# Kernel optimization log

Hardware: AMD Instinct MI355X
Metric: run time of the kernel (lower is better)

## Reference

```python
import jax, jax.numpy as jnp
import numpy as np

B, S, K_IN = 8, 2048, 128
D_MODEL, N_INPUT, N_PROC = 1024, 256, 1024
K_PROC = 256


def setup_inputs() -> dict:
    key = jax.random.key(0)
    k1, k2, k3, k4 = jax.random.split(key, 4)
    selected_input_acts = jax.random.normal(k1, (B, S, K_IN), dtype=jnp.float32)
    input_idx = jax.random.randint(k2, (B, K_IN), 0, N_INPUT)
    # learned params (orthogonal init in torch; random normal is fine for a numeric baseline)
    process_weights = jax.random.normal(k3, (N_PROC, N_INPUT), dtype=jnp.float32) * (2.0 / N_INPUT) ** 0.5
    process_outputs = jax.random.normal(k4, (N_PROC, D_MODEL), dtype=jnp.float32) * (2.0 / N_PROC) ** 0.5
    return {
        "selected_input_acts": selected_input_acts,
        "process_weights": process_weights,
        "process_outputs": process_outputs,
        "input_idx": input_idx,
        "k_process": K_PROC,
    }


def reference(selected_input_acts, process_weights, process_outputs, input_idx, k_process):
    # gather per-batch columns of process_weights: [B, k_input, n_process]
    sel_w = process_weights.T[input_idx]  # (N,P) indexed by (B,k) -> (B,k,P)
    # bmm + exact (erf) gelu, matching torch F.gelu default: [B, S, n_process]
    process_acts = jax.nn.gelu(
        jnp.einsum("bsk,bkp->bsp", selected_input_acts, sel_w),
        approximate=False,
    )
    # router: mean over sequence, top-k process neurons per batch
    process_scores = process_acts.mean(axis=1)  # [B, n_process]
    _, process_idx = jax.lax.top_k(process_scores, k_process)  # [B, k_process]
    # gather selected activations: [B, S, k_process]
    sel_acts = jnp.take_along_axis(process_acts, process_idx[:, None, :], axis=2)
    # gather selected output vectors: [B, k_process, d_model]
    sel_out = process_outputs[process_idx]
    # combine: [B, S, d_model]
    output = jnp.einsum("bsk,bkd->bsd", sel_acts, sel_out)
    return output
```

## Files before the change

kernel.cpp:

```cpp
#include <hip/hip_runtime.h>
#include <hip/hip_bf16.h>

#define NB    8
#define NS    2048
#define NKIN  128
#define NPROC 1024
#define NIN   256
#define NDM   1024
#define NKP   256
#define NSEG  32

typedef unsigned short u16;
typedef unsigned int   u32;
typedef __attribute__((ext_vector_type(4))) u16   u16x4;
typedef __attribute__((ext_vector_type(8))) u16   u16x8;
typedef __attribute__((ext_vector_type(4))) float f32x4;
typedef __attribute__((ext_vector_type(8))) short bf16x8;
typedef __attribute__((ext_vector_type(4))) float f32x4v;

__device__ __forceinline__ float bf2f(u16 u) {
    union { u32 i; float f; } v; v.i = ((u32)u) << 16; return v.f;
}
__device__ __forceinline__ u16 f2bf(float f) {
    u32 x = __float_as_uint(f);
    u32 r = (x + 0x7FFFu + ((x >> 16) & 1u)) >> 16;
    return (u16)r;
}
__device__ __forceinline__ float gelu_fast(float x) {
    float y  = fabsf(x) * 0.70710678118654752f;
    float t  = __builtin_amdgcn_rcpf(fmaf(0.3275911f, y, 1.0f));
    float p  = t * fmaf(t, fmaf(t, fmaf(t, fmaf(t, 1.061405429f,
               -1.453152027f), 1.421413741f), -0.284496736f), 0.254829592f);
    float e  = __expf(-y * y);
    float er = fmaf(-p, e, 1.0f);
    float s  = copysignf(er, x);
    return 0.5f * x * (1.0f + s);
}
__device__ __forceinline__ int clampi(int v, int hi) {
    return v < 0 ? 0 : (v > hi ? hi : v);
}

__global__ __launch_bounds__(256) void k0a_splitA(
        const float* __restrict__ A, u16* __restrict__ AHi,
        u16* __restrict__ ALo) {
    size_t i = ((size_t)blockIdx.x * 256 + threadIdx.x) * 8;
    if (i >= (size_t)NB * NS * NKIN) return;
    f32x4 a = *(const f32x4*)&A[i];
    f32x4 c = *(const f32x4*)&A[i + 4];
    u16x8 h, l;
    #pragma unroll
    for (int j = 0; j < 4; ++j) {
        u16 hj = f2bf(a[j]); h[j] = hj;     l[j]     = f2bf(a[j] - bf2f(hj));
        u16 hk = f2bf(c[j]); h[j + 4] = hk; l[j + 4] = f2bf(c[j] - bf2f(hk));
    }
    *(u16x8*)&AHi[i] = h;
    *(u16x8*)&ALo[i] = l;
}

__global__ __launch_bounds__(256) void k0_prep(
        const float* __restrict__ W, const int* __restrict__ idx,
        u16* __restrict__ WgHi, u16* __restrict__ WgLo) {
    const int b  = blockIdx.x;
    const int p0 = blockIdx.y * 128;
    const int tid = threadIdx.x;
    __shared__ int idxs[NKIN];
    if (tid < NKIN) idxs[tid] = clampi(idx[b * NKIN + tid], NIN - 1);
    __syncthreads();
    for (int e = tid; e < 128 * NKIN; e += 256) {
        int p = p0 + (e >> 7), k = e & 127;
        float x  = W[p * NIN + idxs[k]];
        u16 hi   = f2bf(x);
        u16 lo   = f2bf(x - bf2f(hi));
        size_t o = (size_t)(b * NPROC + p) * NKIN + k;
        WgHi[o] = hi;
        WgLo[o] = lo;
    }
}

__global__ __launch_bounds__(256) void k1_scores(
        const u16* __restrict__ AHi, const u16* __restrict__ ALo,
        const u16* __restrict__ WgHi, const u16* __restrict__ WgLo,
        float* __restrict__ scores, u16* __restrict__ acts) {
    const int lin  = blockIdx.x;
    const int b    = lin & 7;
    const int q    = lin >> 3;
    const int pblk = q & 15;
    const int sblk = q >> 4;
    const int p0 = pblk * 64, s0 = sblk * 64;
    const int tid  = threadIdx.x;
    const int lane = tid & 63;
    const int wid  = tid >> 6;
    const int wr   = wid >> 1;
    const int wc   = wid & 1;

    __shared__ u16  Ah[64 * 64], Al[64 * 64];
    __shared__ u16  Wh[64 * 64], Wl[64 * 64];
    __shared__ float red[2][64];

    f32x4v acc[2][2] = {};

    for (int kc = 0; kc < 2; ++kc) {
        __syncthreads();
        for (int e = tid; e < 512; e += 256) {
            int r = e >> 3, g = e & 7;
            size_t src = (size_t)(b * NS + s0 + r) * NKIN + kc * 64 + g * 8;
            u32 off = (u32)r * 128 + (((u32)g ^ ((u32)r & 7)) << 4);
            *(u16x8*)((char*)Ah + off) = *(const u16x8*)&AHi[src];
            *(u16x8*)((char*)Al + off) = *(const u16x8*)&ALo[src];
        }
        for (int e = tid; e < 512; e += 256) {
            int pp = e >> 3, g = e & 7;
            size_t src = (size_t)(b * NPROC + p0 + pp) * NKIN + kc * 64 + g * 8;
            u32 off = (u32)pp * 128 + (((u32)g ^ ((u32)pp & 7)) << 4);
            *(u16x8*)((char*)Wh + off) = *(const u16x8*)&WgHi[src];
            *(u16x8*)((char*)Wl + off) = *(const u16x8*)&WgLo[src];
        }
        __syncthreads();

        #pragma unroll
        for (int ks = 0; ks < 2; ++ks) {
            const u32 kbyte = (u32)(ks * 64 + (lane >> 4) * 16);
            bf16x8 ah[2], al[2], wh[2], wl[2];
            #pragma unroll
            for (int m = 0; m < 2; ++m) {
                u32 row = (u32)(wr * 32 + m * 16 + (lane & 15));
                u32 off = row * 128 + (kbyte ^ ((row & 7) << 4));
                ah[m] = *(const bf16x8*)((const char*)Ah + off);
                al[m] = *(const bf16x8*)((const char*)Al + off);
            }
            #pragma unroll
            for (int n = 0; n < 2; ++n) {
                u32 col = (u32)(wc * 32 + n * 16 + (lane & 15));
                u32 off = col * 128 + (kbyte ^ ((col & 7) << 4));
                wh[n] = *(const bf16x8*)((const char*)Wh + off);
                wl[n] = *(const bf16x8*)((const char*)Wl + off);
            }
            #pragma unroll
            for (int m = 0; m < 2; ++m)
                #pragma unroll
                for (int n = 0; n < 2; ++n) {
                    acc[m][n] = __builtin_amdgcn_mfma_f32_16x16x32_bf16(
                        ah[m], wh[n], acc[m][n], 0, 0, 0);
                    acc[m][n] = __builtin_amdgcn_mfma_f32_16x16x32_bf16(
                        ah[m], wl[n], acc[m][n], 0, 0, 0);
                    acc[m][n] = __builtin_amdgcn_mfma_f32_16x16x32_bf16(
                        al[m], wh[n], acc[m][n], 0, 0, 0);
                }
        }
    }

    float colsum[2] = {0.f, 0.f};
    #pragma unroll
    for (int n = 0; n < 2; ++n)
        #pragma unroll
        for (int m = 0; m < 2; ++m)
            #pragma unroll
            for (int j = 0; j < 4; ++j) {
                float g = gelu_fast(acc[m][n][j]);
                colsum[n] += g;
                if (acts) {
                    int row = s0 + wr * 32 + m * 16 + (lane >> 4) * 4 + j;
                    int col = p0 + wc * 32 + n * 16 + (lane & 15);
                    acts[(size_t)(b * NS + row) * NPROC + col] = f2bf(g);
                }
            }
    #pragma unroll
    for (int n = 0; n < 2; ++n) {
        colsum[n] += __shfl_xor(colsum[n], 16, 64);
        colsum[n] += __shfl_xor(colsum[n], 32, 64);
    }
    if (lane < 16) {
        #pragma unroll
        for (int n = 0; n < 2; ++n)
            red[wr][wc * 32 + n * 16 + lane] = colsum[n];
    }
    __syncthreads();
    if (tid < 64)
        scores[(size_t)(sblk * NB + b) * NPROC + p0 + tid] =
            red[0][tid] + red[1][tid];
}

__global__ __launch_bounds__(256) void k2_topk(
        const float* __restrict__ scores, int* __restrict__ topk) {
    const int b  = blockIdx.x;
    const int pc = blockIdx.y;
    __shared__ float sc[NPROC];
    #pragma unroll
    for (int q = 0; q < 4; ++q) {
        int p = q * 256 + threadIdx.x;
        float v = 0.f;
        #pragma unroll
        for (int seg = 0; seg < NSEG; ++seg)
            v += scores[(size_t)(seg * NB + b) * NPROC + p];
        sc[p] = v;
    }
    __syncthreads();
    const int p = pc * 256 + threadIdx.x;
    const float v = sc[p];
    int rank = 0;
    #pragma unroll 4
    for (int jj = 0; jj < NPROC / 4; ++jj) {
        f32x4 s4 = *(const f32x4*)&sc[jj * 4];
        #pragma unroll
        for (int c = 0; c < 4; ++c) {
            int j = jj * 4 + c;
            rank += (s4[c] > v) || (s4[c] == v && j < p);
        }
    }
    if (rank < NKP) topk[b * NKP + rank] = p;
}

__global__ __launch_bounds__(256) void k3_gather(
        const u16* __restrict__ acts, const int* __restrict__ topk,
        u16* __restrict__ sel) {
    const int lin   = blockIdx.x;
    const int b     = lin & 7;
    const int q     = lin >> 3;
    const int chalf = q & 1;
    const int sblk  = q >> 1;
    const int c0 = chalf * 128, s0 = sblk * 64;
    const int tid = threadIdx.x;

    __shared__ int tcol[128];
    if (tid < 128) tcol[tid] = clampi(topk[b * NKP + c0 + tid], NPROC - 1);
    __syncthreads();

    const int c     = tid & 127;
    const int rhalf = tid >> 7;
    const int src_c = tcol[c];
    #pragma unroll 8
    for (int r = 0; r < 32; ++r) {
        int row = s0 + rhalf * 32 + r;
        sel[(size_t)(b * NS + row) * NKP + c0 + c] =
            acts[(size_t)(b * NS + row) * NPROC + src_c];
    }
}

__global__ __launch_bounds__(256) void k3_selacts(
        const u16* __restrict__ AHi, const u16* __restrict__ WgHi,
        const int* __restrict__ topk, u16* __restrict__ sel) {
    const int lin  = blockIdx.x;
    const int b    = lin & 7;
    const int q    = lin >> 3;
    const int cblk = q & 3;
    const int sblk = q >> 2;
    const int c0g = cblk * 64, s0 = sblk * 64;
    const int tid  = threadIdx.x;
    const int lane = tid & 63;
    const int wid  = tid >> 6;
    const int wr   = wid >> 1;
    const int wc   = wid & 1;
    const int lr   = lane & 15;
    const int kr   = lane >> 4;

    __shared__ int tcol[64];
    if (tid < 64) tcol[tid] = clampi(topk[b * NKP + c0g + tid], NPROC - 1);
    __syncthreads();

    const u16* ap[2];
    const u16* wp[2];
    #pragma unroll
    for (int m = 0; m < 2; ++m)
        ap[m] = &AHi[(size_t)(b * NS + s0 + wr * 32 + m * 16 + lr) * NKIN + kr * 8];
    #pragma unroll
    for (int n = 0; n < 2; ++n)
        wp[n] = &WgHi[(size_t)(b * NPROC + tcol[wc * 32 + n * 16 + lr]) * NKIN + kr * 8];

    bf16x8 af[2][4], bf[2][4];
    #pragma unroll
    for (int ks = 0; ks < 4; ++ks) {
        #pragma unroll
        for (int m = 0; m < 2; ++m) af[m][ks] = *(const bf16x8*)(ap[m] + ks * 32);
        #pragma unroll
        for (int n = 0; n < 2; ++n) bf[n][ks] = *(const bf16x8*)(wp[n] + ks * 32);
    }

    f32x4v acc[2][2] = {};
    #pragma unroll
    for (int ks = 0; ks < 4; ++ks)
        #pragma unroll
        for (int m = 0; m < 2; ++m)
            #pragma unroll
            for (int n = 0; n < 2; ++n)
                acc[m][n] = __builtin_amdgcn_mfma_f32_16x16x32_bf16(
                    af[m][ks], bf[n][ks], acc[m][n], 0, 0, 0);

    #pragma unroll
    for (int m = 0; m < 2; ++m) {
        const int rbase = s0 + wr * 32 + m * 16 + (lane >> 4) * 4;
        #pragma unroll
        for (int n = 0; n < 2; ++n) {
            const int col = c0g + wc * 32 + n * 16 + lr;
            #pragma unroll
            for (int j = 0; j < 4; ++j)
                sel[(size_t)(b * NS + rbase + j) * NKP + col] =
                    f2bf(gelu_fast(acc[m][n][j]));
        }
    }
}

__global__ __launch_bounds__(256) void k4_mfma(
        const u16* __restrict__ sel, const float* __restrict__ PO,
        const int* __restrict__ topk, float* __restrict__ out) {
    const int lin  = blockIdx.x;
    const int b    = lin & 7;
    const int q    = lin >> 3;
    const int dblk = q & 7;
    const int sblk = q >> 3;
    const int d0 = dblk * 128, s0 = sblk * 128;
    const int tid  = threadIdx.x;
    const int lane = tid & 63;
    const int wid  = tid >> 6;
    const int wr   = wid >> 1;
    const int wc   = wid & 1;

    __shared__ int tloc[NKP];
    __shared__ u16 Alds[128 * 64];
    __shared__ u16 Blds[128 * 64];

    tloc[tid] = clampi(topk[b * NKP + tid], NPROC - 1);

    f32x4v acc[4][4] = {};

    for (int k0 = 0; k0 < NKP; k0 += 64) {
        __syncthreads();
        for (int e = tid; e < 1024; e += 256) {
            int r = e >> 3, g = e & 7;
            u16x8 v = *(const u16x8*)&sel[(size_t)(b * NS + s0 + r) * NKP + k0 + g * 8];
            int slot = g ^ (r & 7);
            *(u16x8*)&Alds[r * 64 + slot * 8] = v;
        }
        for (int e = tid; e < 1024; e += 256) {
            int kp = e >> 5, cg = e & 31;
            f32x4 p0v = *(const f32x4*)&PO[(size_t)tloc[k0 + kp * 2]     * NDM + d0 + cg * 4];
            f32x4 p1v = *(const f32x4*)&PO[(size_t)tloc[k0 + kp * 2 + 1] * NDM + d0 + cg * 4];
            #pragma unroll
            for (int j = 0; j < 4; ++j) {
                int n = cg * 4 + j;
                u32 pack = (u32)f2bf(p0v[j]) | ((u32)f2bf(p1v[j]) << 16);
                u32 byteoff = (u32)n * 128 + (((u32)kp * 4) ^ (((u32)n & 7) << 4));
                *(u32*)((char*)Blds + byteoff) = pack;
            }
        }
        __syncthreads();

        #pragma unroll
        for (int kk = 0; kk < 2; ++kk) {
            const u32 kbase2 = (u32)(kk * 64 + (lane >> 4) * 16);
            bf16x8 afrag[4], bfrag[4];
            #pragma unroll
            for (int m = 0; m < 4; ++m) {
                u32 row = (u32)(wr * 64 + m * 16 + (lane & 15));
                u32 byteoff = row * 128 + (kbase2 ^ ((row & 7) << 4));
                afrag[m] = *(const bf16x8*)((const char*)Alds + byteoff);
            }
            #pragma unroll
            for (int n = 0; n < 4; ++n) {
                u32 col = (u32)(wc * 64 + n * 16 + (lane & 15));
                u32 byteoff = col * 128 + (kbase2 ^ ((col & 7) << 4));
                bfrag[n] = *(const bf16x8*)((const char*)Blds + byteoff);
            }
            #pragma unroll
            for (int m = 0; m < 4; ++m)
                #pragma unroll
                for (int n = 0; n < 4; ++n)
                    acc[m][n] = __builtin_amdgcn_mfma_f32_16x16x32_bf16(
                        afrag[m], bfrag[n], acc[m][n], 0, 0, 0);
        }
    }

    #pragma unroll
    for (int m = 0; m < 4; ++m) {
        const int rbase = s0 + wr * 64 + m * 16 + (lane >> 4) * 4;
        #pragma unroll
        for (int n = 0; n < 4; ++n) {
            const int col = d0 + wc * 64 + n * 16 + (lane & 15);
            #pragma unroll
            for (int j = 0; j < 4; ++j)
                out[(size_t)(b * NS + rbase + j) * NDM + col] = acc[m][n][j];
        }
    }
}

extern "C" void kernel_launch(void* const* d_in, const int* in_sizes, int n_in,
                              void* d_out, int out_size, void* d_ws, size_t ws_size,
                              hipStream_t stream) {
    (void)in_sizes; (void)n_in; (void)out_size;
    const float* A   = (const float*)d_in[0];
    const float* W   = (const float*)d_in[1];
    const float* PO  = (const float*)d_in[2];
    const int*   idx = (const int*)d_in[3];
    float* out = (float*)d_out;

    char* w = (char*)d_ws;
    u16*   sel    = (u16*)w;
    float* scores = (float*)(w + (size_t)8388608);
    int*   topk   = (int*)(w + (size_t)9437184);
    u16*   WgHi   = (u16*)(w + (size_t)9445376);
    u16*   WgLo   = (u16*)(w + (size_t)11542528);
    u16*   AHi    = (u16*)(w + (size_t)13639680);
    u16*   ALo    = (u16*)(w + (size_t)17833984);
    u16*   acts   = (u16*)(w + (size_t)22028288);
    const bool big = ws_size >= (size_t)22028288 + 33554432;

    k0a_splitA<<<1024, 256, 0, stream>>>(A, AHi, ALo);
    k0_prep<<<dim3(NB, NPROC / 128), 256, 0, stream>>>(W, idx, WgHi, WgLo);
    k1_scores<<<4096, 256, 0, stream>>>(AHi, ALo, WgHi, WgLo, scores,
                                        big ? acts : (u16*)nullptr);
    k2_topk<<<dim3(NB, 4), 256, 0, stream>>>(scores, topk);
    if (big)
        k3_gather<<<512, 256, 0, stream>>>(acts, topk, sel);
    else
        k3_selacts<<<1024, 256, 0, stream>>>(AHi, WgHi, topk, sel);
    k4_mfma<<<1024, 256, 0, stream>>>(sel, PO, topk, out);
}
```

Baseline: 118.7 us.

## Merge prep kernels, shrink k1 LDS tiles, stage acts through LDS for coalesced stores

Merges the A split and W gather/split kernels into one launch, which removes one kernel launch and its gap. In the scores kernel, the K loop now uses 32-wide chunks held in a smaller padded LDS pool (80-byte row stride) in place of 64-wide XOR-swizzled tiles. This shrinks LDS per block and may raise occupancy, at the cost of more barriers. The bf16 GELU activations are first written into LDS and then stored to global as 16-byte vectors, replacing scattered 2-byte global writes.

```diff
diff --git a/kernel.cpp b/kernel.cpp
--- a/kernel.cpp
+++ b/kernel.cpp
@@ -40,40 +40,41 @@
     return v < 0 ? 0 : (v > hi ? hi : v);
 }
 
-__global__ __launch_bounds__(256) void k0a_splitA(
-        const float* __restrict__ A, u16* __restrict__ AHi,
-        u16* __restrict__ ALo) {
-    size_t i = ((size_t)blockIdx.x * 256 + threadIdx.x) * 8;
-    if (i >= (size_t)NB * NS * NKIN) return;
-    f32x4 a = *(const f32x4*)&A[i];
-    f32x4 c = *(const f32x4*)&A[i + 4];
-    u16x8 h, l;
-    #pragma unroll
-    for (int j = 0; j < 4; ++j) {
-        u16 hj = f2bf(a[j]); h[j] = hj;     l[j]     = f2bf(a[j] - bf2f(hj));
-        u16 hk = f2bf(c[j]); h[j + 4] = hk; l[j + 4] = f2bf(c[j] - bf2f(hk));
-    }
-    *(u16x8*)&AHi[i] = h;
-    *(u16x8*)&ALo[i] = l;
-}
-
-__global__ __launch_bounds__(256) void k0_prep(
-        const float* __restrict__ W, const int* __restrict__ idx,
-        u16* __restrict__ WgHi, u16* __restrict__ WgLo) {
-    const int b  = blockIdx.x;
-    const int p0 = blockIdx.y * 128;
+__global__ __launch_bounds__(256) void k0_merged(
+        const float* __restrict__ A, const float* __restrict__ W,
+        const int* __restrict__ idx, u16* __restrict__ AHi,
+        u16* __restrict__ ALo, u16* __restrict__ WgHi,
+        u16* __restrict__ WgLo) {
+    const int blk = blockIdx.x;
     const int tid = threadIdx.x;
-    __shared__ int idxs[NKIN];
-    if (tid < NKIN) idxs[tid] = clampi(idx[b * NKIN + tid], NIN - 1);
-    __syncthreads();
-    for (int e = tid; e < 128 * NKIN; e += 256) {
-        int p = p0 + (e >> 7), k = e & 127;
-        float x  = W[p * NIN + idxs[k]];
-        u16 hi   = f2bf(x);
-        u16 lo   = f2bf(x - bf2f(hi));
-        size_t o = (size_t)(b * NPROC + p) * NKIN + k;
-        WgHi[o] = hi;
-        WgLo[o] = lo;
+    if (blk < 1024) {
+        size_t i = ((size_t)blk * 256 + tid) * 8;
+        f32x4 a = *(const f32x4*)&A[i];
+        f32x4 c = *(const f32x4*)&A[i + 4];
+        u16x8 h, l;
+        #pragma unroll
+        for (int j = 0; j < 4; ++j) {
+            u16 hj = f2bf(a[j]); h[j] = hj;     l[j]     = f2bf(a[j] - bf2f(hj));
+            u16 hk = f2bf(c[j]); h[j + 4] = hk; l[j + 4] = f2bf(c[j] - bf2f(hk));
+        }
+        *(u16x8*)&AHi[i] = h;
+        *(u16x8*)&ALo[i] = l;
+    } else {
+        const int q  = blk - 1024;
+        const int b  = q >> 3;
+        const int p0 = (q & 7) * 128;
+        __shared__ int idxs[NKIN];
+        if (tid < NKIN) idxs[tid] = clampi(idx[b * NKIN + tid], NIN - 1);
+        __syncthreads();
+        for (int e = tid; e < 128 * NKIN; e += 256) {
+            int p = p0 + (e >> 7), k = e & 127;
+            float x  = W[p * NIN + idxs[k]];
+            u16 hi   = f2bf(x);
+            u16 lo   = f2bf(x - bf2f(hi));
+            size_t o = (size_t)(b * NPROC + p) * NKIN + k;
+            WgHi[o] = hi;
+            WgLo[o] = lo;
+        }
     }
 }
 
@@ -92,63 +93,63 @@
     const int wid  = tid >> 6;
     const int wr   = wid >> 1;
     const int wc   = wid & 1;
-
-    __shared__ u16  Ah[64 * 64], Al[64 * 64];
-    __shared__ u16  Wh[64 * 64], Wl[64 * 64];
+    const int lr   = lane & 15;
+    const int kr   = lane >> 4;
+
+    __shared__ u16  pool[4 * 64 * 40];
     __shared__ float red[2][64];
+    char* const pb = (char*)pool;
 
     f32x4v acc[2][2] = {};
 
-    for (int kc = 0; kc < 2; ++kc) {
+    for (int kc = 0; kc < 4; ++kc) {
         __syncthreads();
-        for (int e = tid; e < 512; e += 256) {
-            int r = e >> 3, g = e & 7;
-            size_t src = (size_t)(b * NS + s0 + r) * NKIN + kc * 64 + g * 8;
-            u32 off = (u32)r * 128 + (((u32)g ^ ((u32)r & 7)) << 4);
-            *(u16x8*)((char*)Ah + off) = *(const u16x8*)&AHi[src];
-            *(u16x8*)((char*)Al + off) = *(const u16x8*)&ALo[src];
-        }
-        for (int e = tid; e < 512; e += 256) {
-            int pp = e >> 3, g = e & 7;
-            size_t src = (size_t)(b * NPROC + p0 + pp) * NKIN + kc * 64 + g * 8;
-            u32 off = (u32)pp * 128 + (((u32)g ^ ((u32)pp & 7)) << 4);
-            *(u16x8*)((char*)Wh + off) = *(const u16x8*)&WgHi[src];
-            *(u16x8*)((char*)Wl + off) = *(const u16x8*)&WgLo[src];
+        {
+            int r = tid >> 2, g = tid & 3;
+            size_t src = (size_t)(b * NS + s0 + r) * NKIN + kc * 32 + g * 8;
+            u32 off = (u32)r * 80 + (u32)g * 16;
+            *(u16x8*)(pb + off)         = *(const u16x8*)&AHi[src];
+            *(u16x8*)(pb + 5120 + off)  = *(const u16x8*)&ALo[src];
+        }
+        {
+            int pp = tid >> 2, g = tid & 3;
+            size_t src = (size_t)(b * NPROC + p0 + pp) * NKIN + kc * 32 + g * 8;
+            u32 off = (u32)pp * 80 + (u32)g * 16;
+            *(u16x8*)(pb + 10240 + off) = *(const u16x8*)&WgHi[src];
+            *(u16x8*)(pb + 15360 + off) = *(const u16x8*)&WgLo[src];
         }
         __syncthreads();
 
-        #pragma unroll
-        for (int ks = 0; ks < 2; ++ks) {
-            const u32 kbyte = (u32)(ks * 64 + (lane >> 4) * 16);
-            bf16x8 ah[2], al[2], wh[2], wl[2];
-            #pragma unroll
-            for (int m = 0; m < 2; ++m) {
-                u32 row = (u32)(wr * 32 + m * 16 + (lane & 15));
-                u32 off = row * 128 + (kbyte ^ ((row & 7) << 4));
-                ah[m] = *(const bf16x8*)((const char*)Ah + off);
-                al[m] = *(const bf16x8*)((const char*)Al + off);
+        const u32 kb = (u32)kr * 16;
+        bf16x8 ah[2], al[2], wh[2], wl[2];
+        #pragma unroll
+        for (int m = 0; m < 2; ++m) {
+            u32 row = (u32)(wr * 32 + m * 16 + lr);
+            u32 off = row * 80 + kb;
+            ah[m] = *(const bf16x8*)(pb + off);
+            al[m] = *(const bf16x8*)(pb + 5120 + off);
+        }
+        #pragma unroll
+        for (int n = 0; n < 2; ++n) {
+            u32 col = (u32)(wc * 32 + n * 16 + lr);
+            u32 off = col * 80 + kb;
+            wh[n] = *(const bf16x8*)(pb + 10240 + off);
+            wl[n] = *(const bf16x8*)(pb + 15360 + off);
+        }
+        #pragma unroll
+        for (int m = 0; m < 2; ++m)
+            #pragma unroll
+            for (int n = 0; n < 2; ++n) {
+                acc[m][n] = __builtin_amdgcn_mfma_f32_16x16x32_bf16(
+                    ah[m], wh[n], acc[m][n], 0, 0, 0);
+                acc[m][n] = __builtin_amdgcn_mfma_f32_16x16x32_bf16(
+                    ah[m], wl[n], acc[m][n], 0, 0, 0);
+                acc[m][n] = __builtin_amdgcn_mfma_f32_16x16x32_bf16(
+                    al[m], wh[n], acc[m][n], 0, 0, 0);
             }
-            #pragma unroll
-            for (int n = 0; n < 2; ++n) {
-                u32 col = (u32)(wc * 32 + n * 16 + (lane & 15));
-                u32 off = col * 128 + (kbyte ^ ((col & 7) << 4));
-                wh[n] = *(const bf16x8*)((const char*)Wh + off);
-                wl[n] = *(const bf16x8*)((const char*)Wl + off);
-            }
-            #pragma unroll
-            for (int m = 0; m < 2; ++m)
-                #pragma unroll
-                for (int n = 0; n < 2; ++n) {
-                    acc[m][n] = __builtin_amdgcn_mfma_f32_16x16x32_bf16(
-                        ah[m], wh[n], acc[m][n], 0, 0, 0);
-                    acc[m][n] = __builtin_amdgcn_mfma_f32_16x16x32_bf16(
-                        ah[m], wl[n], acc[m][n], 0, 0, 0);
-                    acc[m][n] = __builtin_amdgcn_mfma_f32_16x16x32_bf16(
-                        al[m], wh[n], acc[m][n], 0, 0, 0);
-                }
-        }
-    }
-
+    }
+
+    __syncthreads();
     float colsum[2] = {0.f, 0.f};
     #pragma unroll
     for (int n = 0; n < 2; ++n)
@@ -159,9 +160,9 @@
                 float g = gelu_fast(acc[m][n][j]);
                 colsum[n] += g;
                 if (acts) {
-                    int row = s0 + wr * 32 + m * 16 + (lane >> 4) * 4 + j;
-                    int col = p0 + wc * 32 + n * 16 + (lane & 15);
-                    acts[(size_t)(b * NS + row) * NPROC + col] = f2bf(g);
+                    u32 row = (u32)(wr * 32 + m * 16 + kr * 4 + j);
+                    u32 col = (u32)(wc * 32 + n * 16 + lr);
+                    *(u16*)(pb + row * 128 + col * 2) = f2bf(g);
                 }
             }
     #pragma unroll
@@ -178,6 +179,14 @@
     if (tid < 64)
         scores[(size_t)(sblk * NB + b) * NPROC + p0 + tid] =
             red[0][tid] + red[1][tid];
+    if (acts) {
+        #pragma unroll
+        for (int e = tid; e < 512; e += 256) {
+            int row = e >> 3, g = e & 7;
+            *(u16x8*)&acts[(size_t)(b * NS + s0 + row) * NPROC + p0 + g * 8] =
+                *(const u16x8*)(pb + (u32)row * 128 + (u32)g * 16);
+        }
+    }
 }
 
 __global__ __launch_bounds__(256) void k2_topk(
@@ -403,8 +412,7 @@
     u16*   acts   = (u16*)(w + (size_t)22028288);
     const bool big = ws_size >= (size_t)22028288 + 33554432;
 
-    k0a_splitA<<<1024, 256, 0, stream>>>(A, AHi, ALo);
-    k0_prep<<<dim3(NB, NPROC / 128), 256, 0, stream>>>(W, idx, WgHi, WgLo);
+    k0_merged<<<1024 + 64, 256, 0, stream>>>(A, W, idx, AHi, ALo, WgHi, WgLo);
     k1_scores<<<4096, 256, 0, stream>>>(AHi, ALo, WgHi, WgLo, scores,
                                         big ? acts : (u16*)nullptr);
     k2_topk<<<dim3(NB, 4), 256, 0, stream>>>(scores, topk);
```

Measured after the change: 113.9 us. 4.1% less time.
